# Performance work log

Measured on AMD Instinct MI355X. Metric: run time of the kernel, lower is better.

Reference implementation:

```python
import jax, jax.numpy as jnp
import numpy as np

HEAD_DIM = 256
NUM_HEADS = 8
NUM_KV = 1
MAX_WAVELENGTH = 10000.0


def _apply_rope(x, positions):
    # x: [B, S, N, H], positions: [B, S] int
    d = x.shape[-1]
    freq_exponents = (2.0 / d) * jnp.arange(d // 2, dtype=jnp.float32)
    timescale = MAX_WAVELENGTH ** freq_exponents  # [H/2]
    radians = positions[..., None].astype(jnp.float32) / timescale  # [B, S, H/2]
    radians = radians[..., None, :]  # [B, S, 1, H/2]
    sin, cos = jnp.sin(radians), jnp.cos(radians)
    first, second = jnp.split(x.astype(jnp.float32), 2, axis=-1)
    out = jnp.concatenate([first * cos - second * sin, second * cos + first * sin], axis=-1)
    return out.astype(x.dtype)


def setup_inputs() -> dict:
    key = jax.random.key(0)
    ks = jax.random.split(key, 8)
    B, S0, S1 = 4, 768, 256
    W0, W1 = 2048, 1024
    T = S0 + S1
    s = 0.02  # param init scale
    x0 = jax.random.normal(ks[0], (B, S0, W0), jnp.float32)
    x1 = jax.random.normal(ks[1], (B, S1, W1), jnp.float32)
    w_q0 = jax.random.normal(ks[2], (NUM_HEADS, W0, HEAD_DIM), jnp.float32) * s
    w_kv0 = jax.random.normal(ks[3], (2, NUM_KV, W0, HEAD_DIM), jnp.float32) * s
    w_out0 = jax.random.normal(ks[4], (NUM_HEADS, HEAD_DIM, W0), jnp.float32) * s
    w_q1 = jax.random.normal(ks[5], (NUM_HEADS, W1, HEAD_DIM), jnp.float32) * s
    w_kv1 = jax.random.normal(ks[6], (2, NUM_KV, W1, HEAD_DIM), jnp.float32) * s
    w_out1 = jax.random.normal(ks[7], (NUM_HEADS, HEAD_DIM, W1), jnp.float32) * s
    positions = jnp.broadcast_to(jnp.arange(T, dtype=jnp.int32), (B, T))
    attn_mask = jnp.broadcast_to(jnp.tril(jnp.ones((T, T), bool))[None, None], (B, 1, T, T))
    return {"x0": x0, "x1": x1, "w_q0": w_q0, "w_kv0": w_kv0, "w_out0": w_out0,
            "w_q1": w_q1, "w_kv1": w_kv1, "w_out1": w_out1,
            "positions": positions, "attn_mask": attn_mask}


def reference(x0, x1, w_q0, w_kv0, w_out0, w_q1, w_kv1, w_out1, positions, attn_mask):
    dtype = x0.dtype
    # GQA projections per stream (num_kv_heads != num_heads path)
    q0 = jnp.einsum('BTD,NDH->BTNH', x0, w_q0)
    k0, v0 = jnp.einsum('BSD,CKDH->CBSKH', x0, w_kv0)
    q1 = jnp.einsum('BTD,NDH->BTNH', x1, w_q1)
    k1, v1 = jnp.einsum('BSD,CKDH->CBSKH', x1, w_kv1)
    q = jnp.concatenate([q0, q1], axis=1)  # [B, T, N, H]
    k = jnp.concatenate([k0, k1], axis=1)  # [B, T, K, H]
    v = jnp.concatenate([v0, v1], axis=1)
    q = _apply_rope(q, positions) * (HEAD_DIM ** -0.5)
    k = _apply_rope(k, positions)
    B, T = q.shape[0], q.shape[1]
    G = NUM_HEADS // NUM_KV
    q = q.reshape(B, T, NUM_KV, G, HEAD_DIM)
    logits = jnp.einsum('BTKGH,BSKH->BKGTS', q, k, preferred_element_type=jnp.float32)
    big_neg = -2.3819763e38
    masked = jnp.where(attn_mask[:, :, None, :, :], logits, big_neg)
    probs = jax.nn.softmax(masked, axis=-1).astype(dtype)
    encoded = jnp.einsum('BKGTS,BSKH->BTKGH', probs, v).reshape(B, T, NUM_HEADS, HEAD_DIM)
    S0 = x0.shape[1]
    out0 = jnp.einsum('BTNH,NHD->BTD', encoded[:, :S0], w_out0)
    out1 = jnp.einsum('BTNH,NHD->BTD', encoded[:, S0:], w_out1)
    return (out0, out1, k, v)
```

## Files before the change

kernel.cpp:

```cpp
#include <hip/hip_runtime.h>
#include <hip/hip_bf16.h>

typedef __attribute__((ext_vector_type(8))) short bf16x8;
typedef __attribute__((ext_vector_type(4))) float f32x4;
typedef __attribute__((ext_vector_type(4))) unsigned short u16x4;
typedef unsigned short US;

__device__ __forceinline__ f32x4 mfma16(bf16x8 a, bf16x8 b, f32x4 c) {
  return __builtin_amdgcn_mfma_f32_16x16x32_bf16(a, b, c, 0, 0, 0);
}

__device__ __forceinline__ US f2bf(float f) {
  union { float f; unsigned u; } x; x.f = f;
  unsigned r = x.u + 0x7fffu + ((x.u >> 16) & 1u);
  return (US)(r >> 16);
}

__device__ __forceinline__ void gld16(const US* gp, US* lp) {
  __builtin_amdgcn_global_load_lds(
      (const __attribute__((address_space(1))) unsigned*)gp,
      (__attribute__((address_space(3))) unsigned*)lp, 16, 0, 0);
}

__device__ __forceinline__ int permq(int h) {
  return ((h >> 5) << 6) + (h & 15) + (((h >> 4) & 1) << 5);
}

__device__ __forceinline__ int map_row(int r, int mode) {
  if (mode == 1) { int b = r / 768; return b * 1024 + (r - b * 768); }
  if (mode == 2) { int b = r >> 8; return b * 1024 + 768 + (r & 255); }
  return r;
}

__global__ __launch_bounds__(256)
void k_prep(const float* __restrict__ x0, const float* __restrict__ x1,
            US* __restrict__ x0b, US* __restrict__ x1b,
            const float* __restrict__ wq0, const float* __restrict__ wkv0,
            const float* __restrict__ wq1, const float* __restrict__ wkv1,
            const float* __restrict__ wo0, const float* __restrict__ wo1,
            US* __restrict__ btq0, US* __restrict__ btkv0,
            US* __restrict__ btq1, US* __restrict__ btkv1,
            US* __restrict__ bto0, US* __restrict__ bto1,
            const int* __restrict__ pos, float2* __restrict__ sct) {
  const int bid = blockIdx.x;
  const int tid = threadIdx.x;
  if (bid >= 20992) {
    int idx = (bid - 20992) * 256 + tid;
    int bt = idx >> 7, j = idx & 127;
    float inv_ts = powf(10000.0f, -(float)j * (1.0f / 128.0f));
    float r = (float)pos[bt] * inv_ts;
    sct[idx] = make_float2(sinf(r), cosf(r));
    return;
  }
  if (bid < 7168) {
    const float* src; US* dst; int i;
    if (bid < 6144) { src = x0; dst = x0b; i = bid * 256 + tid; }
    else            { src = x1; dst = x1b; i = (bid - 6144) * 256 + tid; }
    f32x4 v = *reinterpret_cast<const f32x4*>(src + (size_t)i * 4);
    u16x4 o;
    o[0] = f2bf(v[0]); o[1] = f2bf(v[1]); o[2] = f2bf(v[2]); o[3] = f2bf(v[3]);
    *reinterpret_cast<u16x4*>(dst + (size_t)i * 4) = o;
    return;
  }
  __shared__ float tile[32][33];
  const float* src; US* dst; int R, C, CX, local; long sbs, dbs; bool pq = false;
  if (bid < 11264)      { local = bid - 7168;  src = wq0;  dst = btq0;  R = 2048; C = 256;  CX = 8;  sbs = 2048L * 256; dbs = 256L * 2048; pq = true; }
  else if (bid < 12288) { local = bid - 11264; src = wkv0; dst = btkv0; R = 2048; C = 256;  CX = 8;  sbs = 2048L * 256; dbs = 256L * 2048; }
  else if (bid < 14336) { local = bid - 12288; src = wq1;  dst = btq1;  R = 1024; C = 256;  CX = 8;  sbs = 1024L * 256; dbs = 256L * 1024; pq = true; }
  else if (bid < 14848) { local = bid - 14336; src = wkv1; dst = btkv1; R = 1024; C = 256;  CX = 8;  sbs = 1024L * 256; dbs = 256L * 1024; }
  else if (bid < 18944) { local = bid - 14848; src = wo0;  dst = bto0;  R = 2048; C = 2048; CX = 64; sbs = 0; dbs = 0; }
  else                  { local = bid - 18944; src = wo1;  dst = bto1;  R = 2048; C = 1024; CX = 32; sbs = 0; dbs = 0; }
  const int RY = R >> 5;
  const int cx = local % CX;
  const int rest = local / CX;
  const int ry = rest % RY;
  const int z = rest / RY;
  const int c0 = cx * 32, r0 = ry * 32;
  const int tx = tid & 31, ty = tid >> 5;
  src += (long)z * sbs;
  dst += (long)z * dbs;
#pragma unroll
  for (int i = 0; i < 4; ++i)
    tile[ty + 8 * i][tx] = src[(size_t)(r0 + ty + 8 * i) * C + c0 + tx];
  __syncthreads();
#pragma unroll
  for (int i = 0; i < 4; ++i) {
    int h = c0 + ty + 8 * i;
    int ph = pq ? ((h < 128) ? permq(h) : permq(h - 128) + 16) : h;
    dst[(size_t)ph * R + r0 + tx] = f2bf(tile[tx][ty + 8 * i]);
  }
}

__global__ __launch_bounds__(256, 2)
void k_gemm_qkv(const US* __restrict__ x0b, const US* __restrict__ x1b,
                const US* __restrict__ btq0, const US* __restrict__ btq1,
                US* __restrict__ q_bf, float* __restrict__ Ckv,
                const float2* __restrict__ sct) {
  const int bid = blockIdx.x;
  int id = (bid & 7) * 80 + (bid >> 3);
  const US* A; const US* BT; int K, cmap, by, bx;
  if (id < 480) { A = x0b; BT = btq0; K = 2048; cmap = 1; by = id / 20; bx = id % 20; }
  else { id -= 480; A = x1b; BT = btq1; K = 1024; cmap = 2; by = id / 20; bx = id % 20; }

  __shared__ __align__(16) US lA[2][128 * 32];
  __shared__ __align__(16) US lB[2][128 * 32];
  const int tid = threadIdx.x;
  const int lane = tid & 63;
  const int wid = tid >> 6;
  const int wm = wid >> 1, wn = wid & 1;
  const int m0 = by * 128, n0 = bx * 128;
  const int g = lane >> 4, c = lane & 15;
  const int lrow = lane >> 2, lcol = (lane & 3) * 8;
  const size_t ga0 = (size_t)(m0 + wid * 16 + lrow) * K + lcol;
  const size_t ga1 = (size_t)(m0 + 64 + wid * 16 + lrow) * K + lcol;
  const size_t gb0 = (size_t)(n0 + wid * 16 + lrow) * K + lcol;
  const size_t gb1 = (size_t)(n0 + 64 + wid * 16 + lrow) * K + lcol;

  auto stage = [&](int bi, int k0) {
    gld16(A + ga0 + k0, &lA[bi][(wid * 16) * 32]);
    gld16(A + ga1 + k0, &lA[bi][(64 + wid * 16) * 32]);
    gld16(BT + gb0 + k0, &lB[bi][(wid * 16) * 32]);
    gld16(BT + gb1 + k0, &lB[bi][(64 + wid * 16) * 32]);
  };

  f32x4 acc[4][4];
#pragma unroll
  for (int i = 0; i < 4; ++i)
#pragma unroll
    for (int j = 0; j < 4; ++j) acc[i][j] = f32x4{0.f, 0.f, 0.f, 0.f};

  const int nt = K >> 5;
  stage(0, 0);
  __syncthreads();
  for (int t = 0; t < nt; ++t) {
    const int bi = t & 1;
    if (t + 1 < nt) stage(bi ^ 1, (t + 1) * 32);
    bf16x8 af[4], bfr[4];
#pragma unroll
    for (int i = 0; i < 4; ++i) {
      af[i] = *reinterpret_cast<const bf16x8*>(&lA[bi][(wm * 64 + i * 16 + c) * 32 + g * 8]);
      bfr[i] = *reinterpret_cast<const bf16x8*>(&lB[bi][(wn * 64 + i * 16 + c) * 32 + g * 8]);
    }
#pragma unroll
    for (int i = 0; i < 4; ++i)
#pragma unroll
      for (int j = 0; j < 4; ++j)
        acc[i][j] = mfma16(af[i], bfr[j], acc[i][j]);
    __syncthreads();
  }

  const int colb = n0 + wn * 64;
  if (colb < 2048) {
    const int n = colb >> 8;
    const int base64 = colb & 255;
    const int h0 = (base64 >> 6) * 32 + c;
    const float scale = 0.0625f;
#pragma unroll
    for (int i = 0; i < 4; ++i) {
#pragma unroll
      for (int r = 0; r < 4; ++r) {
        const int orow = map_row(m0 + wm * 64 + i * 16 + 4 * g + r, cmap);
        const float2 sc0 = sct[orow * 128 + h0];
        const float2 sc1 = sct[orow * 128 + h0 + 16];
        US* qp = q_bf + ((size_t)orow * 8 + n) * 256 + base64 + c;
        const float q1 = acc[i][0][r], q2 = acc[i][1][r];
        const float q3 = acc[i][2][r], q4 = acc[i][3][r];
        qp[0]  = f2bf(scale * (q1 * sc0.y - q2 * sc0.x));
        qp[16] = f2bf(scale * (q2 * sc0.y + q1 * sc0.x));
        qp[32] = f2bf(scale * (q3 * sc1.y - q4 * sc1.x));
        qp[48] = f2bf(scale * (q4 * sc1.y + q3 * sc1.x));
      }
    }
  } else {
    const int nb = colb - 2048 + c;
#pragma unroll
    for (int i = 0; i < 4; ++i) {
#pragma unroll
      for (int r = 0; r < 4; ++r) {
        const int orow = map_row(m0 + wm * 64 + i * 16 + 4 * g + r, cmap);
        float* cp = Ckv + (size_t)orow * 512 + nb;
#pragma unroll
        for (int j = 0; j < 4; ++j) cp[j * 16] = acc[i][j][r];
      }
    }
  }
}

__global__ __launch_bounds__(256, 2)
void k_gemm_out(const US* __restrict__ A, const US* __restrict__ BT0, const US* __restrict__ BT1,
                float* __restrict__ C0, float* __restrict__ C1) {
  const int bid = blockIdx.x;
  int id = (bid & 7) * 56 + (bid >> 3);
  const US* BT; float* Cb; int amap, mt, ntile, Nst;
  if (id < 384) { amap = 1; mt = id / 16; ntile = id % 16; BT = BT0; Cb = C0; Nst = 2048; }
  else { id -= 384; amap = 2; mt = id / 8; ntile = id % 8; BT = BT1; Cb = C1; Nst = 1024; }
  const int m0 = mt * 128, n0 = ntile * 128;
  const int K = 2048;
  __shared__ __align__(16) US lA[2][128 * 32];
  __shared__ __align__(16) US lB[2][128 * 32];
  const int tid = threadIdx.x;
  const int lane = tid & 63;
  const int wid = tid >> 6;
  const int wm = wid >> 1, wn = wid & 1;
  const int g = lane >> 4, c = lane & 15;
  const int lrow = lane >> 2, lcol = (lane & 3) * 8;
  const size_t ga0 = (size_t)map_row(m0 + wid * 16 + lrow, amap) * K + lcol;
  const size_t ga1 = (size_t)map_row(m0 + 64 + wid * 16 + lrow, amap) * K + lcol;
  const size_t gb0 = (size_t)(n0 + wid * 16 + lrow) * K + lcol;
  const size_t gb1 = (size_t)(n0 + 64 + wid * 16 + lrow) * K + lcol;

  auto stage = [&](int bi, int k0) {
    gld16(A + ga0 + k0, &lA[bi][(wid * 16) * 32]);
    gld16(A + ga1 + k0, &lA[bi][(64 + wid * 16) * 32]);
    gld16(BT + gb0 + k0, &lB[bi][(wid * 16) * 32]);
    gld16(BT + gb1 + k0, &lB[bi][(64 + wid * 16) * 32]);
  };

  f32x4 acc[4][4];
#pragma unroll
  for (int i = 0; i < 4; ++i)
#pragma unroll
    for (int j = 0; j < 4; ++j) acc[i][j] = f32x4{0.f, 0.f, 0.f, 0.f};

  const int nt = K >> 5;
  stage(0, 0);
  __syncthreads();
  for (int t = 0; t < nt; ++t) {
    const int bi = t & 1;
    if (t + 1 < nt) stage(bi ^ 1, (t + 1) * 32);
    bf16x8 af[4], bfr[4];
#pragma unroll
    for (int i = 0; i < 4; ++i) {
      af[i] = *reinterpret_cast<const bf16x8*>(&lA[bi][(wm * 64 + i * 16 + c) * 32 + g * 8]);
      bfr[i] = *reinterpret_cast<const bf16x8*>(&lB[bi][(wn * 64 + i * 16 + c) * 32 + g * 8]);
    }
#pragma unroll
    for (int i = 0; i < 4; ++i)
#pragma unroll
      for (int j = 0; j < 4; ++j)
        acc[i][j] = mfma16(af[i], bfr[j], acc[i][j]);
    __syncthreads();
  }

  const int col = n0 + wn * 64 + c;
#pragma unroll
  for (int i = 0; i < 4; ++i) {
#pragma unroll
    for (int r = 0; r < 4; ++r) {
      const int orow = m0 + wm * 64 + i * 16 + 4 * g + r;
      float* cp = Cb + (size_t)orow * Nst + col;
#pragma unroll
      for (int j = 0; j < 4; ++j) cp[j * 16] = acc[i][j][r];
    }
  }
}

__global__ __launch_bounds__(256)
void k_postkv(const float* __restrict__ kv_raw, const float2* __restrict__ sct,
              US* __restrict__ k_bf, float* __restrict__ k_out,
              float* __restrict__ v_out, US* __restrict__ vt) {
  const int bid = blockIdx.x;
  const int tid = threadIdx.x;
  if (bid >= 1024) {
    const int bt = (bid - 1024) * 2 + (tid >> 7);
    const int j = tid & 127;
    const size_t ko = (size_t)bt * 512;
    const float x1 = kv_raw[ko + j], x2 = kv_raw[ko + j + 128];
    const float2 sc = sct[bt * 128 + j];
    const float o1 = x1 * sc.y - x2 * sc.x, o2 = x2 * sc.y + x1 * sc.x;
    const size_t kd = (size_t)bt * 256;
    const int p = permq(j);
    k_bf[kd + p] = f2bf(o1);
    k_bf[kd + p + 16] = f2bf(o2);
    k_out[kd + j] = o1;
    k_out[kd + j + 128] = o2;
    return;
  }
  __shared__ float tile[32][33];
  const int t0 = (bid & 31) * 32, h0 = ((bid >> 5) & 7) * 32, b = bid >> 8;
  const int tx = tid & 31, ty = tid >> 5;
#pragma unroll
  for (int i = 0; i < 4; ++i) {
    int t = t0 + ty + 8 * i;
    float v = kv_raw[(size_t)(b * 1024 + t) * 512 + 256 + h0 + tx];
    tile[ty + 8 * i][tx] = v;
    v_out[(size_t)(b * 1024 + t) * 256 + h0 + tx] = v;
  }
  __syncthreads();
#pragma unroll
  for (int i = 0; i < 4; ++i) {
    int h = h0 + ty + 8 * i;
    vt[(size_t)(b * 256 + h) * 1024 + t0 + tx] = f2bf(tile[tx][ty + 8 * i]);
  }
}

__global__ __launch_bounds__(256, 2)
void k_attn(const US* __restrict__ qb, const US* __restrict__ kb,
            const US* __restrict__ vt, US* __restrict__ enc) {
  __shared__ __align__(16) US lK[2][32 * 256];
  __shared__ __align__(16) US lV[2][256 * 32];
  const int id = blockIdx.x;
  const int r0_ = (id < 256) ? id : 767 - id;
  const int qt = 63 - (r0_ >> 3);
  const int hg = (r0_ >> 2) & 1;
  const int b = r0_ & 3;
  const int tid = threadIdx.x;
  const int wid = tid >> 6;
  const int lane = tid & 63;
  const int g = lane >> 4, c = lane & 15;
  const int qbase = qt * 16;
  const int n = hg * 4 + wid;

  const US* kbB = kb + (size_t)b * 262144;
  const US* vtB = vt + (size_t)b * 262144;

  bf16x8 qf[8];
  {
    const US* qp = qb + ((size_t)((b * 1024 + qbase + c) * 8 + n)) * 256 + 8 * g;
#pragma unroll
    for (int ch = 0; ch < 8; ++ch)
      qf[ch] = *reinterpret_cast<const bf16x8*>(qp + ch * 32);
  }

  auto stage = [&](int bi, int c0) {
#pragma unroll
    for (int j = 0; j < 4; ++j) {
      const int rk = wid * 8 + j * 2 + (lane >> 5);
      const int sk = lane & 31;
      gld16(kbB + (size_t)(c0 + rk) * 256 + (sk ^ (rk & 7)) * 8,
            &lK[bi][(wid * 8 + j * 2) * 256]);
      const int rv = wid * 64 + j * 16 + (lane >> 2);
      const int sv = lane & 3;
      gld16(vtB + (size_t)rv * 1024 + c0 + (sv ^ ((rv >> 1) & 3)) * 8,
            &lV[bi][(wid * 64 + j * 16) * 32]);
    }
  };

  f32x4 acc[16];
#pragma unroll
  for (int i = 0; i < 16; ++i) acc[i] = f32x4{0.f, 0.f, 0.f, 0.f};
  float m_run = -3.0e38f, l_run = 0.f;

  const int nC = qbase / 32 + 1;
  stage(0, 0);
  __syncthreads();

  for (int i = 0; i < nC; ++i) {
    const int c0 = 32 * i;
    const int bi = i & 1;
    if (i + 1 < nC) stage(bi ^ 1, c0 + 32);

    const bool hb = (c0 + 16 <= qbase);
    f32x4 sA = {0.f, 0.f, 0.f, 0.f}, sB = {0.f, 0.f, 0.f, 0.f};
    __builtin_amdgcn_s_setprio(1);
#pragma unroll
    for (int ch = 0; ch < 8; ++ch) {
      const int slot = (((ch * 4 + g) ^ (c & 7)) * 8);
      sA = mfma16(*reinterpret_cast<const bf16x8*>(&lK[bi][c * 256 + slot]), qf[ch], sA);
    }
    if (hb) {
#pragma unroll
      for (int ch = 0; ch < 8; ++ch) {
        const int slot = (((ch * 4 + g) ^ (c & 7)) * 8);
        sB = mfma16(*reinterpret_cast<const bf16x8*>(&lK[bi][(c + 16) * 256 + slot]), qf[ch], sB);
      }
    }
    __builtin_amdgcn_s_setprio(0);
    if (c0 == qbase) {
#pragma unroll
      for (int r = 0; r < 4; ++r)
        if (4 * g + r > c) sA[r] = -3.0e38f;
    }
    if (hb && (c0 + 16 == qbase)) {
#pragma unroll
      for (int r = 0; r < 4; ++r)
        if (4 * g + r > c) sB[r] = -3.0e38f;
    }
    float tm = fmaxf(fmaxf(sA[0], sA[1]), fmaxf(sA[2], sA[3]));
    if (hb) tm = fmaxf(tm, fmaxf(fmaxf(sB[0], sB[1]), fmaxf(sB[2], sB[3])));
    tm = fmaxf(tm, __shfl_xor(tm, 16));
    tm = fmaxf(tm, __shfl_xor(tm, 32));
    if (!__all(tm - m_run <= 8.0f)) {
      const float m_new = fmaxf(m_run, tm);
      const float alpha = __expf(m_run - m_new);
      float aacc[4];
#pragma unroll
      for (int r = 0; r < 4; ++r) aacc[r] = __shfl(alpha, 4 * g + r);
#pragma unroll
      for (int ht = 0; ht < 16; ++ht) {
        acc[ht][0] *= aacc[0]; acc[ht][1] *= aacc[1];
        acc[ht][2] *= aacc[2]; acc[ht][3] *= aacc[3];
      }
      l_run *= alpha;
      m_run = m_new;
    }
    float pA[4], pB[4];
    float ls = 0.f;
#pragma unroll
    for (int r = 0; r < 4; ++r) { pA[r] = __expf(sA[r] - m_run); ls += pA[r]; }
#pragma unroll
    for (int r = 0; r < 4; ++r) { pB[r] = hb ? __expf(sB[r] - m_run) : 0.f; ls += pB[r]; }
    ls += __shfl_xor(ls, 16);
    ls += __shfl_xor(ls, 32);
    l_run += ls;

    unsigned w0, w1, w2, w3;
    asm("v_cvt_pk_bf16_f32 %0, %1, %2" : "=v"(w0) : "v"(pA[0]), "v"(pA[1]));
    asm("v_cvt_pk_bf16_f32 %0, %1, %2" : "=v"(w1) : "v"(pA[2]), "v"(pA[3]));
    asm("v_cvt_pk_bf16_f32 %0, %1, %2" : "=v"(w2) : "v"(pB[0]), "v"(pB[1]));
    asm("v_cvt_pk_bf16_f32 %0, %1, %2" : "=v"(w3) : "v"(pB[2]), "v"(pB[3]));
    const bool bb1 = ((g >> 1) & 1) != 0, bb0 = (g & 1) != 0;
    unsigned ownA = bb1 ? w2 : w0, ownB = bb1 ? w3 : w1;
    unsigned sndA = bb1 ? w0 : w2, sndB = bb1 ? w1 : w3;
    unsigned rcvA = (unsigned)__shfl_xor((int)sndA, 32);
    unsigned rcvB = (unsigned)__shfl_xor((int)sndB, 32);
    unsigned kA = (bb0 == bb1) ? ownA : rcvA, kB = (bb0 == bb1) ? ownB : rcvB;
    unsigned s2A = (bb0 == bb1) ? rcvA : ownA, s2B = (bb0 == bb1) ? rcvB : ownB;
    unsigned gA = (unsigned)__shfl_xor((int)s2A, 16);
    unsigned gB = (unsigned)__shfl_xor((int)s2B, 16);
    union { unsigned u[4]; bf16x8 v; } pu;
    pu.u[0] = bb0 ? gA : kA; pu.u[1] = bb0 ? gB : kB;
    pu.u[2] = bb0 ? kA : gA; pu.u[3] = bb0 ? kB : gB;
    const bf16x8 paf = pu.v;

    __builtin_amdgcn_s_setprio(1);
#pragma unroll
    for (int ht = 0; ht < 16; ++ht) {
      const int h = ht * 16 + c;
      const int slot = (g ^ ((c >> 1) & 3)) * 8;
      bf16x8 vf = *reinterpret_cast<const bf16x8*>(&lV[bi][h * 32 + slot]);
      acc[ht] = mfma16(paf, vf, acc[ht]);
    }
    __builtin_amdgcn_s_setprio(0);
    __syncthreads();
  }

  const float inv = 1.0f / l_run;
  float ia[4];
#pragma unroll
  for (int r = 0; r < 4; ++r) ia[r] = __shfl(inv, 4 * g + r);
#pragma unroll
  for (int ht = 0; ht < 16; ++ht) {
#pragma unroll
    for (int r = 0; r < 4; ++r) {
      size_t o = ((size_t)((b * 1024 + qbase + 4 * g + r) * 8 + n)) * 256 + ht * 16 + c;
      enc[o] = f2bf(acc[ht][r] * ia[r]);
    }
  }
}

extern "C" void kernel_launch(void* const* d_in, const int* in_sizes, int n_in,
                              void* d_out, int out_size, void* d_ws, size_t ws_size,
                              hipStream_t stream) {
  const float* x0 = (const float*)d_in[0];
  const float* x1 = (const float*)d_in[1];
  const float* wq0 = (const float*)d_in[2];
  const float* wkv0 = (const float*)d_in[3];
  const float* wo0 = (const float*)d_in[4];
  const float* wq1 = (const float*)d_in[5];
  const float* wkv1 = (const float*)d_in[6];
  const float* wo1 = (const float*)d_in[7];
  const int* pos = (const int*)d_in[8];
  float* out = (float*)d_out;

  float* out0 = out;
  float* out1 = out + 6291456;
  float* k_out = out + 7340032;
  float* v_out = out + 8388608;

  char* ws = (char*)d_ws;
  size_t off = 0;
  auto alloc = [&](size_t bytes) {
    char* p = ws + off;
    off += (bytes + 255) & ~(size_t)255;
    return p;
  };
  US* x0b   = (US*)alloc(6291456ull * 2);
  US* x1b   = (US*)alloc(1048576ull * 2);
  US* btq0  = (US*)alloc(2048ull * 2048 * 2);
  US* btkv0 = (US*)alloc(512ull * 2048 * 2);
  US* btq1  = (US*)alloc(2048ull * 1024 * 2);
  US* btkv1 = (US*)alloc(512ull * 1024 * 2);
  US* bto0  = (US*)alloc(2048ull * 2048 * 2);
  US* bto1  = (US*)alloc(1024ull * 2048 * 2);
  float* kv_raw = (float*)alloc(2097152ull * 4);
  US* q_bf = (US*)alloc(8388608ull * 2);
  US* k_bf = (US*)alloc(1048576ull * 2);
  US* vt   = (US*)alloc(1048576ull * 2 + 256);
  US* enc  = (US*)alloc(8388608ull * 2);
  float2* sct = (float2*)alloc(524288ull * 8);
  (void)btkv0; (void)btkv1;

  k_prep<<<23040, 256, 0, stream>>>(x0, x1, x0b, x1b, wq0, wkv0, wq1, wkv1, wo0, wo1,
                                    btq0, btkv0, btq1, btkv1, bto0, bto1, pos, sct);

  k_gemm_qkv<<<640, 256, 0, stream>>>(x0b, x1b, btq0, btq1, q_bf, kv_raw, sct);

  k_postkv<<<3072, 256, 0, stream>>>(kv_raw, sct, k_bf, k_out, v_out, vt);

  k_attn<<<512, 256, 0, stream>>>(q_bf, k_bf, vt, enc);

  k_gemm_out<<<448, 256, 0, stream>>>(enc, bto0, bto1, out0, out1);
}
```

Baseline: 194.5 us.

## Move output-weight transpose/convert into attention launch as extra blocks

The fp32-to-bf16 transpose of the output projection weights moves out of the prep kernel and into the attention kernel as 6144 extra tail blocks (ids >= 512). The aim is to let this memory-bound work fill CUs left idle by the 512 attention blocks instead of running serially in prep. The extra blocks reuse the K shared-memory buffer as the transpose tile. Because they share the attention kernel's launch bounds and LDS allocation, they may run at limited occupancy, and their scheduling relative to the attention blocks is up to the hardware.

```diff
diff --git a/kernel.cpp b/kernel.cpp
--- a/kernel.cpp
+++ b/kernel.cpp
@@ -37,15 +37,13 @@
             US* __restrict__ x0b, US* __restrict__ x1b,
             const float* __restrict__ wq0, const float* __restrict__ wkv0,
             const float* __restrict__ wq1, const float* __restrict__ wkv1,
-            const float* __restrict__ wo0, const float* __restrict__ wo1,
             US* __restrict__ btq0, US* __restrict__ btkv0,
             US* __restrict__ btq1, US* __restrict__ btkv1,
-            US* __restrict__ bto0, US* __restrict__ bto1,
             const int* __restrict__ pos, float2* __restrict__ sct) {
   const int bid = blockIdx.x;
   const int tid = threadIdx.x;
-  if (bid >= 20992) {
-    int idx = (bid - 20992) * 256 + tid;
+  if (bid >= 14848) {
+    int idx = (bid - 14848) * 256 + tid;
     int bt = idx >> 7, j = idx & 127;
     float inv_ts = powf(10000.0f, -(float)j * (1.0f / 128.0f));
     float r = (float)pos[bt] * inv_ts;
@@ -64,12 +62,10 @@
   }
   __shared__ float tile[32][33];
   const float* src; US* dst; int R, C, CX, local; long sbs, dbs; bool pq = false;
-  if (bid < 11264)      { local = bid - 7168;  src = wq0;  dst = btq0;  R = 2048; C = 256;  CX = 8;  sbs = 2048L * 256; dbs = 256L * 2048; pq = true; }
-  else if (bid < 12288) { local = bid - 11264; src = wkv0; dst = btkv0; R = 2048; C = 256;  CX = 8;  sbs = 2048L * 256; dbs = 256L * 2048; }
-  else if (bid < 14336) { local = bid - 12288; src = wq1;  dst = btq1;  R = 1024; C = 256;  CX = 8;  sbs = 1024L * 256; dbs = 256L * 1024; pq = true; }
-  else if (bid < 14848) { local = bid - 14336; src = wkv1; dst = btkv1; R = 1024; C = 256;  CX = 8;  sbs = 1024L * 256; dbs = 256L * 1024; }
-  else if (bid < 18944) { local = bid - 14848; src = wo0;  dst = bto0;  R = 2048; C = 2048; CX = 64; sbs = 0; dbs = 0; }
-  else                  { local = bid - 18944; src = wo1;  dst = bto1;  R = 2048; C = 1024; CX = 32; sbs = 0; dbs = 0; }
+  if (bid < 11264)      { local = bid - 7168;  src = wq0;  dst = btq0;  R = 2048; C = 256; CX = 8; sbs = 2048L * 256; dbs = 256L * 2048; pq = true; }
+  else if (bid < 12288) { local = bid - 11264; src = wkv0; dst = btkv0; R = 2048; C = 256; CX = 8; sbs = 2048L * 256; dbs = 256L * 2048; }
+  else if (bid < 14336) { local = bid - 12288; src = wq1;  dst = btq1;  R = 1024; C = 256; CX = 8; sbs = 1024L * 256; dbs = 256L * 1024; pq = true; }
+  else                  { local = bid - 14336; src = wkv1; dst = btkv1; R = 1024; C = 256; CX = 8; sbs = 1024L * 256; dbs = 256L * 1024; }
   const int RY = R >> 5;
   const int cx = local % CX;
   const int rest = local / CX;
@@ -296,15 +292,37 @@
 
 __global__ __launch_bounds__(256, 2)
 void k_attn(const US* __restrict__ qb, const US* __restrict__ kb,
-            const US* __restrict__ vt, US* __restrict__ enc) {
+            const US* __restrict__ vt, US* __restrict__ enc,
+            const float* __restrict__ wo0, const float* __restrict__ wo1,
+            US* __restrict__ bto0, US* __restrict__ bto1) {
   __shared__ __align__(16) US lK[2][32 * 256];
   __shared__ __align__(16) US lV[2][256 * 32];
   const int id = blockIdx.x;
+  const int tid = threadIdx.x;
+
+  if (id >= 512) {
+    int local = id - 512;
+    const float* src; US* dst; int C, CX;
+    if (local < 4096) { src = wo0; dst = bto0; C = 2048; CX = 64; }
+    else { local -= 4096; src = wo1; dst = bto1; C = 1024; CX = 32; }
+    const int cx = local % CX, ry = local / CX;
+    const int c0p = cx * 32, r0p = ry * 32;
+    const int tx = tid & 31, ty = tid >> 5;
+    float* tileF = (float*)&lK[0][0];
+#pragma unroll
+    for (int i = 0; i < 4; ++i)
+      tileF[(ty + 8 * i) * 33 + tx] = src[(size_t)(r0p + ty + 8 * i) * C + c0p + tx];
+    __syncthreads();
+#pragma unroll
+    for (int i = 0; i < 4; ++i)
+      dst[(size_t)(c0p + ty + 8 * i) * 2048 + r0p + tx] = f2bf(tileF[tx * 33 + ty + 8 * i]);
+    return;
+  }
+
   const int r0_ = (id < 256) ? id : 767 - id;
   const int qt = 63 - (r0_ >> 3);
   const int hg = (r0_ >> 2) & 1;
   const int b = r0_ & 3;
-  const int tid = threadIdx.x;
   const int wid = tid >> 6;
   const int lane = tid & 63;
   const int g = lane >> 4, c = lane & 15;
@@ -491,14 +509,14 @@
   float2* sct = (float2*)alloc(524288ull * 8);
   (void)btkv0; (void)btkv1;
 
-  k_prep<<<23040, 256, 0, stream>>>(x0, x1, x0b, x1b, wq0, wkv0, wq1, wkv1, wo0, wo1,
-                                    btq0, btkv0, btq1, btkv1, bto0, bto1, pos, sct);
+  k_prep<<<16896, 256, 0, stream>>>(x0, x1, x0b, x1b, wq0, wkv0, wq1, wkv1,
+                                    btq0, btkv0, btq1, btkv1, pos, sct);
 
   k_gemm_qkv<<<640, 256, 0, stream>>>(x0b, x1b, btq0, btq1, q_bf, kv_raw, sct);
 
   k_postkv<<<3072, 256, 0, stream>>>(kv_raw, sct, k_bf, k_out, v_out, vt);
 
-  k_attn<<<512, 256, 0, stream>>>(q_bf, k_bf, vt, enc);
+  k_attn<<<6656, 256, 0, stream>>>(q_bf, k_bf, vt, enc, wo0, wo1, bto0, bto1);
 
   k_gemm_out<<<448, 256, 0, stream>>>(enc, bto0, bto1, out0, out1);
 }
```

New measurement: 190.5 us. 1.02x faster.
